# Optimization experiments

Hardware: AMD Instinct MI355X
Metric: run time of the kernel (lower is better)

## Reference

```python
import jax, jax.numpy as jnp
from jax import lax
import numpy as np
import itertools

KD, NH, D, WS = 16, 8, 32, 7  # key_dim, num_heads, value dim per head, window size
SCALE = KD ** -0.5


def _affine(y, s, b):
    # eval-mode BatchNorm folded to per-channel scale/shift
    return y * s[:, None, None] + b[:, None, None]


def _conv1x1(x, w, s, b):
    return _affine(jnp.einsum('bchw,oc->bohw', x, w), s, b)


def _dwconv(x, w, s, b, pad):
    # w: (C, k, k) depthwise kernel
    y = lax.conv_general_dilated(x, w[:, None], (1, 1), [(pad, pad), (pad, pad)],
                                 feature_group_count=x.shape[1],
                                 dimension_numbers=('NCHW', 'OIHW', 'NCHW'))
    return _affine(y, s, b)


def _ffn(x, w1, s1, b1, w2, s2, b2):
    return _conv1x1(jax.nn.relu(_conv1x1(x, w1, s1, b1)), w2, s2, b2)


def _bias_idxs(res):
    pts = list(itertools.product(range(res), range(res)))
    offs, idxs = {}, []
    for p1 in pts:
        for p2 in pts:
            o = (abs(p1[0] - p2[0]), abs(p1[1] - p2[1]))
            if o not in offs:
                offs[o] = len(offs)
            idxs.append(offs[o])
    n = len(pts)
    return np.array(idxs, dtype=np.int32).reshape(n, n), len(offs)


def setup_inputs() -> dict:
    key = jax.random.key(0)
    ks = jax.random.split(key, 40)
    B, C, H, W = 128, 256, 28, 28
    hid = 2 * C
    qkv_out = 2 * KD + D  # 96
    idxs, n_off = _bias_idxs(WS)

    def w_(k, shape):
        return jax.random.normal(k, shape, jnp.float32) * 0.02

    def s_(k, c):
        return 1.0 + jax.random.normal(k, (c,), jnp.float32) * 0.05

    def b_(k, c):
        return jax.random.normal(k, (c,), jnp.float32) * 0.05

    inp = {'x': jax.random.normal(ks[0], (B, C, H, W), jnp.float32)}
    inp['dw0_w'] = w_(ks[1], (C, 3, 3)); inp['dw0_s'] = s_(ks[2], C); inp['dw0_b'] = b_(ks[3], C)
    inp['ffn0_w1'] = w_(ks[4], (hid, C)); inp['ffn0_s1'] = s_(ks[5], hid); inp['ffn0_b1'] = b_(ks[6], hid)
    inp['ffn0_w2'] = w_(ks[7], (C, hid)); inp['ffn0_s2'] = s_(ks[8], C); inp['ffn0_b2'] = b_(ks[9], C)
    inp['qkv_w'] = w_(ks[10], (NH, qkv_out, C // NH)); inp['qkv_s'] = s_(ks[11], NH * qkv_out).reshape(NH, qkv_out); inp['qkv_b'] = b_(ks[12], NH * qkv_out).reshape(NH, qkv_out)
    inp['dwq_w'] = w_(ks[13], (NH, KD, 5, 5)); inp['dwq_s'] = s_(ks[14], NH * KD).reshape(NH, KD); inp['dwq_b'] = b_(ks[15], NH * KD).reshape(NH, KD)
    inp['attn_biases'] = jax.random.normal(ks[16], (NH, n_off), jnp.float32) * 0.02
    inp['proj_w'] = w_(ks[17], (C, NH * D)); inp['proj_s'] = s_(ks[18], C); inp['proj_b'] = b_(ks[19], C)
    inp['dw1_w'] = w_(ks[20], (C, 3, 3)); inp['dw1_s'] = s_(ks[21], C); inp['dw1_b'] = b_(ks[22], C)
    inp['ffn1_w1'] = w_(ks[23], (hid, C)); inp['ffn1_s1'] = s_(ks[24], hid); inp['ffn1_b1'] = b_(ks[25], hid)
    inp['ffn1_w2'] = w_(ks[26], (C, hid)); inp['ffn1_s2'] = s_(ks[27], C); inp['ffn1_b2'] = b_(ks[28], C)
    inp['bias_idxs'] = jnp.asarray(idxs)
    return inp


def reference(x, dw0_w, dw0_s, dw0_b, ffn0_w1, ffn0_s1, ffn0_b1, ffn0_w2, ffn0_s2, ffn0_b2,
              qkv_w, qkv_s, qkv_b, dwq_w, dwq_s, dwq_b, attn_biases, proj_w, proj_s, proj_b,
              dw1_w, dw1_s, dw1_b, ffn1_w1, ffn1_s1, ffn1_b1, ffn1_w2, ffn1_s2, ffn1_b2, bias_idxs):
    B, C, H, W = x.shape
    nH, nW = H // WS, W // WS
    N = WS * WS

    x = x + _dwconv(x, dw0_w, dw0_s, dw0_b, 1)
    x = x + _ffn(x, ffn0_w1, ffn0_s1, ffn0_b1, ffn0_w2, ffn0_s2, ffn0_b2)

    # window partition: (B,C,H,W) -> (B*nH*nW, C, WS, WS)
    xw = x.reshape(B, C, nH, WS, nW, WS).transpose(0, 2, 4, 1, 3, 5).reshape(B * nH * nW, C, WS, WS)
    Bw = xw.shape[0]

    ab = attn_biases[:, bias_idxs]  # (NH, N, N)
    feats_in = xw.reshape(Bw, NH, C // NH, WS, WS)
    feat = feats_in[:, 0]
    outs = []
    for i in range(NH):
        if i > 0:
            feat = feat + feats_in[:, i]
        f = _conv1x1(feat, qkv_w[i], qkv_s[i], qkv_b[i])  # (Bw, 96, WS, WS)
        q, k, v = f[:, :KD], f[:, KD:2 * KD], f[:, 2 * KD:]
        q = _dwconv(q, dwq_w[i], dwq_s[i], dwq_b[i], 2)
        qf, kf, vf = q.reshape(Bw, KD, N), k.reshape(Bw, KD, N), v.reshape(Bw, D, N)
        attn = jnp.einsum('bdn,bdm->bnm', qf, kf) * SCALE + ab[i]
        attn = jax.nn.softmax(attn, axis=-1)
        feat = jnp.einsum('bdm,bnm->bdn', vf, attn).reshape(Bw, D, WS, WS)
        outs.append(feat)
    y = jnp.concatenate(outs, axis=1)  # (Bw, NH*D, WS, WS)
    y = _conv1x1(jax.nn.relu(y), proj_w, proj_s, proj_b)

    # window reverse
    y = y.reshape(B, nH, nW, C, WS, WS).transpose(0, 3, 1, 4, 2, 5).reshape(B, C, H, W)
    x = x + y

    x = x + _dwconv(x, dw1_w, dw1_s, dw1_b, 1)
    x = x + _ffn(x, ffn1_w1, ffn1_s1, ffn1_b1, ffn1_w2, ffn1_s2, ffn1_b2)
    return x
```

## Files before the change

### kernel.cpp

```cpp
#include <hip/hip_runtime.h>
#include <hip/hip_bf16.h>

using bf16 = __hip_bfloat16;
using short8 = __attribute__((ext_vector_type(8))) short;
using f32x4  = __attribute__((ext_vector_type(4))) float;

#define BATCH 128
#define CCH   256
#define HWSZ  784
#define NPOS  100352
#define NWIN  2048

__device__ __forceinline__ ushort f2u(float f) {
    bf16 h = __float2bfloat16(f);
    return *reinterpret_cast<ushort*>(&h);
}
__device__ __forceinline__ float u2f(ushort u) {
    bf16 h;
    *reinterpret_cast<ushort*>(&h) = u;
    return __bfloat162float(h);
}
__device__ __forceinline__ int swz64(int row, int col) {
    return row * 64 + (col ^ ((row & 7) << 3));
}
__device__ __forceinline__ void gl_lds16(const void* g, void* l) {
    __builtin_amdgcn_global_load_lds(
        (const __attribute__((address_space(1))) void*)g,
        (__attribute__((address_space(3))) void*)l, 16, 0, 0);
}

__global__ __launch_bounds__(256) void wcvt_k(const float* __restrict__ w1a,
                                              const float* __restrict__ w2a,
                                              const float* __restrict__ pw,
                                              const float* __restrict__ w1b,
                                              const float* __restrict__ w2b,
                                              const float* __restrict__ qw,
                                              const float* __restrict__ qs,
                                              const float* __restrict__ qbi,
                                              const float* __restrict__ dqw,
                                              const float* __restrict__ dqs,
                                              const float* __restrict__ dqb,
                                              ushort* __restrict__ out) {
    int i = blockIdx.x * 256 + threadIdx.x;
    if (i >= 610048) return;
    float v;
    if (i < 131072)      v = w1a[i];
    else if (i < 262144) v = w2a[i - 131072];
    else if (i < 327680) v = pw[i - 262144];
    else if (i < 458752) v = w1b[i - 327680];
    else if (i < 589824) v = w2b[i - 458752];
    else if (i < 606208) { int j = i - 589824; v = qs[j >> 5] * qw[j]; }
    else if (i < 609408) { int j = i - 606208; v = dqs[j / 25] * dqw[j]; }
    else if (i < 609920) v = qbi[i - 609408];
    else                 v = dqb[i - 609920];
    out[i] = f2u(v);
}

__global__ __launch_bounds__(256) void abx_k(const float* __restrict__ ab,
                                             const int* __restrict__ bidx,
                                             float* __restrict__ abx) {
    int i = blockIdx.x * 256 + threadIdx.x;
    if (i >= 8 * 2401) return;
    int h = i / 2401, r = i - h * 2401;
    abx[i] = ab[h * 49 + bidx[r]];
}

__global__ __launch_bounds__(256) void tin_k(const float* __restrict__ X,
                                             ushort* __restrict__ O) {
    __shared__ ushort tile[256][113];
    const int pc = blockIdx.x, b = blockIdx.y;
    const int t = threadIdx.x;
    const size_t xbase = (size_t)b * 256 * 784 + pc * 112;
    for (int r = 0; r < 112; ++r) {
        int idx = r * 256 + t;
        int c = idx / 112, p = idx - c * 112;
        tile[c][p] = f2u(X[xbase + (size_t)c * 784 + p]);
    }
    __syncthreads();
    const size_t obase = ((size_t)b * 784 + pc * 112) * 256;
    for (int r = 0; r < 112; ++r) {
        int idx = r * 256 + t;
        int p = idx >> 8, c = idx & 255;
        O[obase + (size_t)p * 256 + c] = tile[c][p];
    }
}

__global__ __launch_bounds__(256) void dw3n_k(const ushort* __restrict__ X,
                                              const float* __restrict__ Wg,
                                              const float* __restrict__ sc,
                                              const float* __restrict__ bi,
                                              ushort* __restrict__ O) {
    const int h = blockIdx.x, b = blockIdx.y;
    const int c = threadIdx.x;
    float wv[9];
#pragma unroll
    for (int k = 0; k < 9; ++k) wv[k] = Wg[c * 9 + k];
    const float s = sc[c], bb = bi[c];
    const size_t base = (size_t)b * 784 * 256;
    for (int w = 0; w < 28; ++w) {
        float acc = 0.f, ctr = 0.f;
#pragma unroll
        for (int dh = -1; dh <= 1; ++dh) {
            int hh = h + dh;
            if (hh < 0 || hh >= 28) continue;
#pragma unroll
            for (int dw = -1; dw <= 1; ++dw) {
                int ww = w + dw;
                if (ww < 0 || ww >= 28) continue;
                float xv = u2f(X[base + (size_t)(hh * 28 + ww) * 256 + c]);
                if (dh == 0 && dw == 0) ctr = xv;
                acc += wv[(dh + 1) * 3 + (dw + 1)] * xv;
            }
        }
        O[base + (size_t)(h * 28 + w) * 256 + c] = f2u(ctr + s * acc + bb);
    }
}

template <int IC, int OC, bool RELU_OUT, bool RESID, bool NCHW_OUT>
__global__ __launch_bounds__(256) void gemm_k(const ushort* __restrict__ X,
                                              const ushort* __restrict__ Wb,
                                              const float* __restrict__ sc,
                                              const float* __restrict__ bi,
                                              const ushort* __restrict__ res,
                                              void* __restrict__ outp) {
    __shared__ ushort As[128 * 32];
    __shared__ ushort Bs[128 * 32];
    const int t = threadIdx.x;
    const int pos0 = blockIdx.x * 128;
    const int oc0  = blockIdx.y * 128;
    const int wave = t >> 6, lane = t & 63;
    const int qd = lane >> 4, ln = lane & 15;
    const int pw = (wave >> 1) * 64, ow = (wave & 1) * 64;
    const int grow = lane >> 2;
    const int gcol = ((lane & 3) ^ ((lane >> 3) & 3)) * 8;
    const int xsl = (qd ^ ((ln >> 1) & 3)) * 8;

    f32x4 acc[4][4];
#pragma unroll
    for (int i = 0; i < 4; ++i)
#pragma unroll
        for (int j = 0; j < 4; ++j) acc[i][j] = (f32x4)0.f;

    for (int k0 = 0; k0 < IC; k0 += 32) {
        __syncthreads();
#pragma unroll
        for (int r = 0; r < 2; ++r) {
            const int rowbase = wave * 16 + r * 64;
            gl_lds16(&X[(size_t)(pos0 + rowbase + grow) * IC + k0 + gcol],
                     &As[rowbase * 32]);
            gl_lds16(&Wb[(size_t)(oc0 + rowbase + grow) * IC + k0 + gcol],
                     &Bs[rowbase * 32]);
        }
        __syncthreads();
        short8 bfr[4];
#pragma unroll
        for (int j = 0; j < 4; ++j)
            bfr[j] = *(const short8*)&Bs[(ow + j * 16 + ln) * 32 + xsl];
#pragma unroll
        for (int i = 0; i < 4; ++i) {
            short8 a = *(const short8*)&As[(pw + i * 16 + ln) * 32 + xsl];
#pragma unroll
            for (int j = 0; j < 4; ++j)
                acc[i][j] = __builtin_amdgcn_mfma_f32_16x16x32_bf16(a, bfr[j], acc[i][j], 0, 0, 0);
        }
    }

#pragma unroll
    for (int j = 0; j < 4; ++j) {
        const int oc = oc0 + ow + j * 16 + ln;
        const float s = sc[oc], bb = bi[oc];
#pragma unroll
        for (int i = 0; i < 4; ++i) {
#pragma unroll
            for (int r = 0; r < 4; ++r) {
                const int pos = pos0 + pw + i * 16 + qd * 4 + r;
                float v = s * acc[i][j][r] + bb;
                if constexpr (RELU_OUT) v = fmaxf(v, 0.f);
                if constexpr (RESID) v += u2f(res[(size_t)pos * 256 + oc]);
                if constexpr (NCHW_OUT) {
                    int bb2 = pos / 784, hw = pos - bb2 * 784;
                    ((float*)outp)[((size_t)bb2 * 256 + oc) * 784 + hw] = v;
                } else {
                    ((ushort*)outp)[(size_t)pos * OC + oc] = f2u(v);
                }
            }
        }
    }
}

__global__ __launch_bounds__(256, 4) void attn_k(const ushort* __restrict__ X,
                                                 const ushort* __restrict__ qwb,
                                                 const ushort* __restrict__ qbb,
                                                 const ushort* __restrict__ dwvb,
                                                 const ushort* __restrict__ dbbb,
                                                 const float* __restrict__ abx,
                                                 ushort* __restrict__ Y) {
    __shared__ ushort featB[64 * 32];
    __shared__ ushort q2t[64 * 32];
    __shared__ ushort kt[64 * 32];
    __shared__ ushort vd[32 * 64];
    __shared__ ushort pt[64 * 64];
    __shared__ float  uni[16 * 121];
    __shared__ ushort dwv[3200];
    __shared__ ushort qb[512];
    __shared__ ushort dbl[128];
    __shared__ int    posmap[49];
    __shared__ int    puni[49];

    const int t = threadIdx.x;
    const int w = blockIdx.x;
    const int b = w >> 4, wh = (w >> 2) & 3, ww = w & 3;
    const int wv_ = t >> 6, lane = t & 63;
    const int ln = lane & 15, qd = lane >> 4;
    const int msl = (ln >> 1) & 3;
    const int fsl = (qd ^ msl) * 8;

    if (t < 49) {
        int pi = t / 7, pj = t - pi * 7;
        posmap[t] = b * 784 + (wh * 7 + pi) * 28 + ww * 7 + pj;
        puni[t] = (pi + 2) * 11 + (pj + 2);
    }
    for (int i = t; i < 16 * 121; i += 256) uni[i] = 0.f;
    for (int i = t; i < 64 * 32; i += 256) { q2t[i] = 0; kt[i] = 0; featB[i] = 0; }
    for (int i = t; i < 32 * 64; i += 256) vd[i] = 0;
    for (int i = t; i < 64 * 64; i += 256) pt[i] = 0;
    for (int i = t; i < 3200; i += 256) dwv[i] = dwvb[i];
    for (int i = t; i < 512; i += 256) qb[i] = qbb[i];
    if (t < 128) dbl[t] = dbbb[t];
    for (int i = t; i < 1568; i += 256) {
        int p = i >> 5, c = i & 31;
        int pi = p / 7, pj = p - pi * 7;
        featB[p * 32 + (c & 7) + (((c >> 3) ^ ((p >> 1) & 3)) << 3)] =
            X[(size_t)(b * 784 + (wh * 7 + pi) * 28 + ww * 7 + pj) * 256 + c];
    }
    __syncthreads();

    const int arow = (16 * wv_ + ln) * 32 + fsl;

    for (int head = 0; head < 8; ++head) {
        {
            short8 afr = *(const short8*)&qwb[head * 2048 + (16 * wv_ + ln) * 32 + qd * 8];
            f32x4 acc[4];
#pragma unroll
            for (int j = 0; j < 4; ++j) acc[j] = (f32x4)0.f;
#pragma unroll
            for (int j = 0; j < 4; ++j) {
                short8 bfr = *(const short8*)&featB[(16 * j + ln) * 32 + fsl];
                acc[j] = __builtin_amdgcn_mfma_f32_16x16x32_bf16(afr, bfr, acc[j], 0, 0, 0);
            }
            float qbv[4];
#pragma unroll
            for (int r = 0; r < 4; ++r)
                qbv[r] = u2f(qb[head * 64 + 16 * wv_ + qd * 4 + r]);
#pragma unroll
            for (int j = 0; j < 4; ++j) {
                int p = 16 * j + ln;
                if (p >= 49) continue;
                if (wv_ == 0) {
                    int pu = puni[p];
#pragma unroll
                    for (int r = 0; r < 4; ++r)
                        uni[(qd * 4 + r) * 121 + pu] = acc[j][r] + qbv[r];
                } else if (wv_ == 1) {
#pragma unroll
                    for (int r = 0; r < 4; ++r)
                        kt[p * 32 + ((qd * 4 + r) & 7) + ((((qd >> 1)) ^ msl) << 3)] =
                            f2u(acc[j][r] + qbv[r]);
                } else {
#pragma unroll
                    for (int r = 0; r < 4; ++r)
                        vd[swz64((wv_ - 2) * 16 + qd * 4 + r, p)] =
                            f2u(acc[j][r] + qbv[r]);
                }
            }
        }
        __syncthreads();

        {
            const int d = ln;
            float tap[25];
#pragma unroll
            for (int u = 0; u < 25; ++u)
                tap[u] = u2f(dwv[head * 400 + d * 25 + u]);
            float db = u2f(dbl[head * 16 + d]);
#pragma unroll
            for (int k = 0; k < 4; ++k) {
                int p = 16 * wv_ + k * 4 + qd;
                int mq = (2 * k + (qd >> 1)) & 3;
                if (p < 49) {
                    const float* qp = &uni[d * 121 + (puni[p] - 24)];
                    float a = 0.f;
#pragma unroll
                    for (int u = 0; u < 5; ++u)
#pragma unroll
                        for (int v5 = 0; v5 < 5; ++v5)
                            a += tap[u * 5 + v5] * qp[u * 11 + v5];
                    q2t[p * 32 + (d & 7) + (((d >> 3) ^ mq) << 3)] = f2u(a + db);
                }
            }
        }

        {
            short8 afr = *(const short8*)&q2t[arow];
            f32x4 acc[4];
#pragma unroll
            for (int j = 0; j < 4; ++j) acc[j] = (f32x4)0.f;
#pragma unroll
            for (int j = 0; j < 4; ++j) {
                short8 bfr = *(const short8*)&kt[(16 * j + ln) * 32 + fsl];
                acc[j] = __builtin_amdgcn_mfma_f32_16x16x32_bf16(afr, bfr, acc[j], 0, 0, 0);
            }
            const int nbase = 16 * wv_ + qd * 4;
            float lg[4][4];
#pragma unroll
            for (int j = 0; j < 4; ++j) {
                int m = 16 * j + ln;
#pragma unroll
                for (int r = 0; r < 4; ++r) {
                    int n = nbase + r;
                    if (n < 49 && m < 49)
                        lg[j][r] = acc[j][r] * 0.25f + abx[head * 2401 + n * 49 + m];
                    else
                        lg[j][r] = -3e38f;
                }
            }
            float mx[4], sm[4];
#pragma unroll
            for (int r = 0; r < 4; ++r)
                mx[r] = fmaxf(fmaxf(lg[0][r], lg[1][r]), fmaxf(lg[2][r], lg[3][r]));
#pragma unroll
            for (int s = 1; s <= 8; s <<= 1)
#pragma unroll
                for (int r = 0; r < 4; ++r)
                    mx[r] = fmaxf(mx[r], __shfl_xor(mx[r], s, 16));
#pragma unroll
            for (int r = 0; r < 4; ++r) sm[r] = 0.f;
#pragma unroll
            for (int j = 0; j < 4; ++j) {
                int m = 16 * j + ln;
#pragma unroll
                for (int r = 0; r < 4; ++r) {
                    float e = __expf(lg[j][r] - mx[r]);
                    sm[r] += e;
                    int n = nbase + r;
                    if (n < 49 && m < 49) pt[swz64(n, m)] = f2u(e);
                }
            }
#pragma unroll
            for (int s = 1; s <= 8; s <<= 1)
#pragma unroll
                for (int r = 0; r < 4; ++r)
                    sm[r] += __shfl_xor(sm[r], s, 16);
            float inv[4];
#pragma unroll
            for (int r = 0; r < 4; ++r) inv[r] = 1.f / sm[r];

            f32x4 av[2];
            av[0] = (f32x4)0.f; av[1] = (f32x4)0.f;
#pragma unroll
            for (int ks = 0; ks < 2; ++ks) {
                const int cs = (ks * 32 + qd * 8) ^ ((ln & 7) << 3);
                short8 pa = *(const short8*)&pt[(16 * wv_ + ln) * 64 + cs];
#pragma unroll
                for (int dt = 0; dt < 2; ++dt) {
                    short8 vb = *(const short8*)&vd[(16 * dt + ln) * 64 + cs];
                    av[dt] = __builtin_amdgcn_mfma_f32_16x16x32_bf16(pa, vb, av[dt], 0, 0, 0);
                }
            }
#pragma unroll
            for (int r = 0; r < 4; ++r) {
                int n = nbase + r;
                if (n >= 49) continue;
                size_t pbase = (size_t)posmap[n] * 256;
                int mn = (2 * qd + (r >> 1)) & 3;
#pragma unroll
                for (int dt = 0; dt < 2; ++dt) {
                    int c = 16 * dt + ln;
                    float val = av[dt][r] * inv[r];
                    Y[pbase + head * 32 + c] = f2u(fmaxf(val, 0.f));
                    if (head < 7)
                        featB[n * 32 + (ln & 7) +
                              (((2 * dt + (ln >> 3)) ^ mn) << 3)] =
                            f2u(val + u2f(X[pbase + (head + 1) * 32 + c]));
                }
            }
        }
        __syncthreads();
    }
}

extern "C" void kernel_launch(void* const* d_in, const int* in_sizes, int n_in,
                              void* d_out, int out_size, void* d_ws, size_t ws_size,
                              hipStream_t stream) {
    const float* x       = (const float*)d_in[0];
    const float* dw0_w   = (const float*)d_in[1];
    const float* dw0_s   = (const float*)d_in[2];
    const float* dw0_b   = (const float*)d_in[3];
    const float* ffn0_w1 = (const float*)d_in[4];
    const float* ffn0_s1 = (const float*)d_in[5];
    const float* ffn0_b1 = (const float*)d_in[6];
    const float* ffn0_w2 = (const float*)d_in[7];
    const float* ffn0_s2 = (const float*)d_in[8];
    const float* ffn0_b2 = (const float*)d_in[9];
    const float* qkv_w   = (const float*)d_in[10];
    const float* qkv_s   = (const float*)d_in[11];
    const float* qkv_b   = (const float*)d_in[12];
    const float* dwq_w   = (const float*)d_in[13];
    const float* dwq_s   = (const float*)d_in[14];
    const float* dwq_b   = (const float*)d_in[15];
    const float* attn_b  = (const float*)d_in[16];
    const float* proj_w  = (const float*)d_in[17];
    const float* proj_s  = (const float*)d_in[18];
    const float* proj_b  = (const float*)d_in[19];
    const float* dw1_w   = (const float*)d_in[20];
    const float* dw1_s   = (const float*)d_in[21];
    const float* dw1_b   = (const float*)d_in[22];
    const float* ffn1_w1 = (const float*)d_in[23];
    const float* ffn1_s1 = (const float*)d_in[24];
    const float* ffn1_b1 = (const float*)d_in[25];
    const float* ffn1_w2 = (const float*)d_in[26];
    const float* ffn1_s2 = (const float*)d_in[27];
    const float* ffn1_b2 = (const float*)d_in[28];
    const int*   bidx    = (const int*)d_in[29];

    char* ws = (char*)d_ws;
    const size_t NEL = (size_t)NPOS * 256;
    ushort* wbf = (ushort*)ws;
    float*  abx = (float*)(ws + 1220096);
    ushort* U0 = (ushort*)(ws + 1220096 + 76832);
    ushort* U1 = U0 + NEL;
    ushort* U2 = U1 + NEL;
    ushort* H  = U2 + NEL;
    const ushort* w1a_b = wbf;
    const ushort* w2a_b = wbf + 131072;
    const ushort* prj_b = wbf + 262144;
    const ushort* w1b_b = wbf + 327680;
    const ushort* w2b_b = wbf + 458752;
    const ushort* qwb   = wbf + 589824;
    const ushort* dwvb  = wbf + 606208;
    const ushort* qbb   = wbf + 609408;
    const ushort* dbbb  = wbf + 609920;

    wcvt_k<<<2383, 256, 0, stream>>>(ffn0_w1, ffn0_w2, proj_w, ffn1_w1, ffn1_w2,
                                     qkv_w, qkv_s, qkv_b, dwq_w, dwq_s, dwq_b, wbf);
    abx_k<<<76, 256, 0, stream>>>(attn_b, bidx, abx);
    tin_k<<<dim3(7, BATCH), 256, 0, stream>>>(x, U0);
    dw3n_k<<<dim3(28, BATCH), 256, 0, stream>>>(U0, dw0_w, dw0_s, dw0_b, U1);
    gemm_k<256, 512, true, false, false>
        <<<dim3(784, 4), 256, 0, stream>>>(U1, w1a_b, ffn0_s1, ffn0_b1, nullptr, H);
    gemm_k<512, 256, false, true, false>
        <<<dim3(784, 2), 256, 0, stream>>>(H, w2a_b, ffn0_s2, ffn0_b2, U1, U2);
    attn_k<<<NWIN, 256, 0, stream>>>(U2, qwb, qbb, dwvb, dbbb, abx, U0);
    gemm_k<256, 256, false, true, false>
        <<<dim3(784, 2), 256, 0, stream>>>(U0, prj_b, proj_s, proj_b, U2, U1);
    dw3n_k<<<dim3(28, BATCH), 256, 0, stream>>>(U1, dw1_w, dw1_s, dw1_b, U2);
    gemm_k<256, 512, true, false, false>
        <<<dim3(784, 4), 256, 0, stream>>>(U2, w1b_b, ffn1_s1, ffn1_b1, nullptr, H);
    gemm_k<512, 256, false, true, true>
        <<<dim3(784, 2), 256, 0, stream>>>(H, w2b_b, ffn1_s2, ffn1_b2, U2, d_out);
}
```

Before: 960.8 us.

## Double-buffer GEMM LDS tiles and prefetch attention bias and residual loads

The 1x1-conv GEMM kernel now uses two LDS buffers so the global-to-LDS copy of the next K tile is issued before the MFMAs on the current tile, with one barrier per iteration instead of two. The attention kernel now loads the relative-position bias and the next head's input slice into registers at the start of each head loop, so those global loads overlap the QKV and depthwise work. The cost is twice the LDS for the GEMM tiles, which can lower occupancy, plus higher register pressure in the attention kernel.

```diff
diff --git a/kernel.cpp b/kernel.cpp
--- a/kernel.cpp
+++ b/kernel.cpp
@@ -123,8 +123,8 @@
                                               const float* __restrict__ bi,
                                               const ushort* __restrict__ res,
                                               void* __restrict__ outp) {
-    __shared__ ushort As[128 * 32];
-    __shared__ ushort Bs[128 * 32];
+    __shared__ ushort As[2][128 * 32];
+    __shared__ ushort Bs[2][128 * 32];
     const int t = threadIdx.x;
     const int pos0 = blockIdx.x * 128;
     const int oc0  = blockIdx.y * 128;
@@ -141,28 +141,42 @@
 #pragma unroll
         for (int j = 0; j < 4; ++j) acc[i][j] = (f32x4)0.f;
 
-    for (int k0 = 0; k0 < IC; k0 += 32) {
-        __syncthreads();
-#pragma unroll
-        for (int r = 0; r < 2; ++r) {
-            const int rowbase = wave * 16 + r * 64;
-            gl_lds16(&X[(size_t)(pos0 + rowbase + grow) * IC + k0 + gcol],
-                     &As[rowbase * 32]);
-            gl_lds16(&Wb[(size_t)(oc0 + rowbase + grow) * IC + k0 + gcol],
-                     &Bs[rowbase * 32]);
-        }
-        __syncthreads();
+    constexpr int NT = IC / 32;
+#pragma unroll
+    for (int r = 0; r < 2; ++r) {
+        const int rowbase = wave * 16 + r * 64;
+        gl_lds16(&X[(size_t)(pos0 + rowbase + grow) * IC + gcol], &As[0][rowbase * 32]);
+        gl_lds16(&Wb[(size_t)(oc0 + rowbase + grow) * IC + gcol], &Bs[0][rowbase * 32]);
+    }
+    __syncthreads();
+
+    int cur = 0;
+#pragma unroll
+    for (int kt = 0; kt < NT; ++kt) {
+        if (kt + 1 < NT) {
+            const int k0 = (kt + 1) * 32;
+#pragma unroll
+            for (int r = 0; r < 2; ++r) {
+                const int rowbase = wave * 16 + r * 64;
+                gl_lds16(&X[(size_t)(pos0 + rowbase + grow) * IC + k0 + gcol],
+                         &As[cur ^ 1][rowbase * 32]);
+                gl_lds16(&Wb[(size_t)(oc0 + rowbase + grow) * IC + k0 + gcol],
+                         &Bs[cur ^ 1][rowbase * 32]);
+            }
+        }
         short8 bfr[4];
 #pragma unroll
         for (int j = 0; j < 4; ++j)
-            bfr[j] = *(const short8*)&Bs[(ow + j * 16 + ln) * 32 + xsl];
+            bfr[j] = *(const short8*)&Bs[cur][(ow + j * 16 + ln) * 32 + xsl];
 #pragma unroll
         for (int i = 0; i < 4; ++i) {
-            short8 a = *(const short8*)&As[(pw + i * 16 + ln) * 32 + xsl];
+            short8 a = *(const short8*)&As[cur][(pw + i * 16 + ln) * 32 + xsl];
 #pragma unroll
             for (int j = 0; j < 4; ++j)
                 acc[i][j] = __builtin_amdgcn_mfma_f32_16x16x32_bf16(a, bfr[j], acc[i][j], 0, 0, 0);
         }
+        __syncthreads();
+        cur ^= 1;
     }
 
 #pragma unroll
@@ -214,6 +228,7 @@
     const int ln = lane & 15, qd = lane >> 4;
     const int msl = (ln >> 1) & 3;
     const int fsl = (qd ^ msl) * 8;
+    const int nbase = 16 * wv_ + qd * 4;
 
     if (t < 49) {
         int pi = t / 7, pj = t - pi * 7;
@@ -238,6 +253,29 @@
     const int arow = (16 * wv_ + ln) * 32 + fsl;
 
     for (int head = 0; head < 8; ++head) {
+        float bias[4][4];
+#pragma unroll
+        for (int j = 0; j < 4; ++j) {
+            int m = 16 * j + ln;
+#pragma unroll
+            for (int r = 0; r < 4; ++r) {
+                int n = nbase + r;
+                bias[j][r] = (n < 49 && m < 49) ? abx[head * 2401 + n * 49 + m] : 0.f;
+            }
+        }
+        ushort xnx[4][2];
+#pragma unroll
+        for (int r = 0; r < 4; ++r) {
+            int n = nbase + r;
+            if (head < 7 && n < 49) {
+#pragma unroll
+                for (int dt = 0; dt < 2; ++dt)
+                    xnx[r][dt] = X[(size_t)posmap[n] * 256 + (head + 1) * 32 + 16 * dt + ln];
+            } else {
+                xnx[r][0] = 0; xnx[r][1] = 0;
+            }
+        }
+
         {
             short8 afr = *(const short8*)&qwb[head * 2048 + (16 * wv_ + ln) * 32 + qd * 8];
             f32x4 acc[4];
@@ -310,7 +348,6 @@
                 short8 bfr = *(const short8*)&kt[(16 * j + ln) * 32 + fsl];
                 acc[j] = __builtin_amdgcn_mfma_f32_16x16x32_bf16(afr, bfr, acc[j], 0, 0, 0);
             }
-            const int nbase = 16 * wv_ + qd * 4;
             float lg[4][4];
 #pragma unroll
             for (int j = 0; j < 4; ++j) {
@@ -319,7 +356,7 @@
                 for (int r = 0; r < 4; ++r) {
                     int n = nbase + r;
                     if (n < 49 && m < 49)
-                        lg[j][r] = acc[j][r] * 0.25f + abx[head * 2401 + n * 49 + m];
+                        lg[j][r] = acc[j][r] * 0.25f + bias[j][r];
                     else
                         lg[j][r] = -3e38f;
                 }
@@ -381,7 +418,7 @@
                     if (head < 7)
                         featB[n * 32 + (ln & 7) +
                               (((2 * dt + (ln >> 3)) ^ mn) << 3)] =
-                            f2u(val + u2f(X[pbase + (head + 1) * 32 + c]));
+                            f2u(val + u2f(xnx[r][dt]));
                 }
             }
         }
```

New measurement: 1.019 ms. +6.1%, slower.

## Double-buffer LDS tiles in 1x1-conv GEMM to overlap global loads with MFMA

Applied to the files above, without the earlier changes.

Splits the shared A/B tiles into two buffers and prefetches the next K-slice with direct global-to-LDS loads while MFMAs run on the current slice. Explicit vmcnt waits and scheduling barriers replace the two __syncthreads per iteration, so global latency can hide behind compute. This doubles LDS use per block, which may lower occupancy, and depends on hand-counted outstanding-load numbers being correct.

```diff
diff --git a/kernel.cpp b/kernel.cpp
--- a/kernel.cpp
+++ b/kernel.cpp
@@ -123,8 +123,8 @@
                                               const float* __restrict__ bi,
                                               const ushort* __restrict__ res,
                                               void* __restrict__ outp) {
-    __shared__ ushort As[128 * 32];
-    __shared__ ushort Bs[128 * 32];
+    __shared__ ushort As[2][128 * 32];
+    __shared__ ushort Bs[2][128 * 32];
     const int t = threadIdx.x;
     const int pos0 = blockIdx.x * 128;
     const int oc0  = blockIdx.y * 128;
@@ -141,28 +141,49 @@
 #pragma unroll
         for (int j = 0; j < 4; ++j) acc[i][j] = (f32x4)0.f;
 
-    for (int k0 = 0; k0 < IC; k0 += 32) {
-        __syncthreads();
-#pragma unroll
-        for (int r = 0; r < 2; ++r) {
-            const int rowbase = wave * 16 + r * 64;
-            gl_lds16(&X[(size_t)(pos0 + rowbase + grow) * IC + k0 + gcol],
-                     &As[rowbase * 32]);
-            gl_lds16(&Wb[(size_t)(oc0 + rowbase + grow) * IC + k0 + gcol],
-                     &Bs[rowbase * 32]);
-        }
-        __syncthreads();
+    constexpr int NT = IC / 32;
+#pragma unroll
+    for (int r = 0; r < 2; ++r) {
+        const int rowbase = wave * 16 + r * 64;
+        gl_lds16(&X[(size_t)(pos0 + rowbase + grow) * IC + gcol], &As[0][rowbase * 32]);
+        gl_lds16(&Wb[(size_t)(oc0 + rowbase + grow) * IC + gcol], &Bs[0][rowbase * 32]);
+    }
+
+    for (int kt = 0; kt < NT; ++kt) {
+        const int cur = kt & 1;
+        if (kt + 1 < NT) {
+            const int k0 = (kt + 1) * 32;
+#pragma unroll
+            for (int r = 0; r < 2; ++r) {
+                const int rowbase = wave * 16 + r * 64;
+                gl_lds16(&X[(size_t)(pos0 + rowbase + grow) * IC + k0 + gcol],
+                         &As[cur ^ 1][rowbase * 32]);
+                gl_lds16(&Wb[(size_t)(oc0 + rowbase + grow) * IC + k0 + gcol],
+                         &Bs[cur ^ 1][rowbase * 32]);
+            }
+            asm volatile("s_waitcnt vmcnt(4)" ::: "memory");
+        } else {
+            asm volatile("s_waitcnt vmcnt(0)" ::: "memory");
+        }
+        __builtin_amdgcn_sched_barrier(0);
+        __builtin_amdgcn_s_barrier();
+        __builtin_amdgcn_sched_barrier(0);
+
         short8 bfr[4];
 #pragma unroll
         for (int j = 0; j < 4; ++j)
-            bfr[j] = *(const short8*)&Bs[(ow + j * 16 + ln) * 32 + xsl];
+            bfr[j] = *(const short8*)&Bs[cur][(ow + j * 16 + ln) * 32 + xsl];
 #pragma unroll
         for (int i = 0; i < 4; ++i) {
-            short8 a = *(const short8*)&As[(pw + i * 16 + ln) * 32 + xsl];
+            short8 a = *(const short8*)&As[cur][(pw + i * 16 + ln) * 32 + xsl];
 #pragma unroll
             for (int j = 0; j < 4; ++j)
                 acc[i][j] = __builtin_amdgcn_mfma_f32_16x16x32_bf16(a, bfr[j], acc[i][j], 0, 0, 0);
         }
+        __builtin_amdgcn_sched_barrier(0);
+        asm volatile("s_waitcnt lgkmcnt(0)" ::: "memory");
+        __builtin_amdgcn_s_barrier();
+        __builtin_amdgcn_sched_barrier(0);
     }
 
 #pragma unroll
```

Result: no change. 965.9 us (+0.5%).
